# Kernel optimization log

Hardware: AMD Instinct MI355X
Metric: run time of the kernel (lower is better)

## Reference

```python
import jax, jax.numpy as jnp
import numpy as np

# HRR ops (holoformer): bind = circular convolution via FFT; unbind = circular
# correlation (bind with the approximate inverse), i.e. conj in freq domain.

def _fft(a):
    return jnp.fft.fft(a, axis=-1)

def _bind_f(Fa, Fb):
    return jnp.fft.ifft(Fa * Fb, axis=-1).real

def _unbind_f(Fs, Fk):
    return jnp.fft.ifft(Fs * jnp.conj(Fk), axis=-1).real


def setup_inputs() -> dict:
    key = jax.random.key(0)
    B, S, D = 4, 4096, 1024
    ks = jax.random.split(key, 5)
    scale = 1.0 / np.sqrt(D)
    inp = {
        "x": jax.random.normal(ks[0], (B, S, D), dtype=jnp.float32),
        "Wq": jax.random.normal(ks[1], (D, D), dtype=jnp.float32) * scale,
        "bq": jnp.zeros((D,), jnp.float32),
        "Wk": jax.random.normal(ks[2], (D, D), dtype=jnp.float32) * scale,
        "bk": jnp.zeros((D,), jnp.float32),
        "Wv": jax.random.normal(ks[3], (D, D), dtype=jnp.float32) * scale,
        "bv": jnp.zeros((D,), jnp.float32),
        "Wr": jax.random.normal(ks[4], (D, D), dtype=jnp.float32) * scale,
        "br": jnp.zeros((D,), jnp.float32),
    }
    return inp


def reference(x, Wq, bq, Wk, bk, Wv, bv, Wr, br):
    # tanh-gated linear projections (nn.Linear stores weight as [out, in])
    query = jnp.tanh(jnp.einsum('bsd,ed->bse', x, Wq) + bq)
    keys = jnp.tanh(jnp.einsum('bsd,ed->bse', x, Wk) + bk)
    values = jnp.tanh(jnp.einsum('bsd,ed->bse', x, Wv) + bv)
    remove_query = jnp.tanh(jnp.einsum('bsd,ed->bse', x, Wr) + br)

    # bind(keys, values) and sum over sequence -> s: (B, 1, D)
    x_k = _bind_f(_fft(keys), _fft(values))
    s = x_k.sum(axis=1, keepdims=True)
    Fs = _fft(s)

    # retrieve with query, add
    retrieved = _unbind_f(Fs, _fft(query))
    out = x + retrieved

    # remove: bind(remove_query, unbind(s, remove_query))
    Fr = _fft(remove_query)
    remove_values = _unbind_f(Fs, Fr)
    removes = _bind_f(Fr, _fft(remove_values))
    out = out - removes
    return out
```

## Files before the change

kernel.cpp:

```cpp
#include <hip/hip_runtime.h>
#include <hip/hip_fp16.h>

#define D 1024
#define LOG2D 10
#define S_LEN 4096
#define BATCH 4
#define NROWS (BATCH * S_LEN)
#define PI_F 3.14159265358979323846f

#define SLOT(p) ((p) + ((p) >> 4))
#define FBUF 1088
#define NTW 341

typedef _Float16 f16x8 __attribute__((ext_vector_type(8)));
typedef float f32x4 __attribute__((ext_vector_type(4)));

__device__ __forceinline__ float2 cmul(float2 a, float2 b) {
    return make_float2(a.x * b.x - a.y * b.y, a.x * b.y + a.y * b.x);
}

__device__ __forceinline__ float fast_tanh(float v) {
    float e = __expf(2.0f * v);
    return 1.0f - 2.0f * __builtin_amdgcn_rcpf(e + 1.0f);
}

__device__ __forceinline__ void g2lds16(const void* g, void* l) {
    __builtin_amdgcn_global_load_lds(
        (const __attribute__((address_space(1))) unsigned int*)g,
        (__attribute__((address_space(3))) unsigned int*)l, 16, 0, 0);
}

__global__ __launch_bounds__(256) void convert_all(
    const float* __restrict__ x,
    const float* __restrict__ w0, const float* __restrict__ w1,
    const float* __restrict__ w2, const float* __restrict__ w3,
    __half* __restrict__ xh,
    __half* __restrict__ h0, __half* __restrict__ h1,
    __half* __restrict__ h2, __half* __restrict__ h3)
{
    const int b = blockIdx.x;
    const float* s;
    __half* d;
    int li;
    if (b < 16384) { s = x; d = xh; li = b; }
    else {
        int t = b - 16384;
        int r = t >> 10;
        li = t & 1023;
        s = (r == 0) ? w0 : (r == 1) ? w1 : (r == 2) ? w2 : w3;
        d = (r == 0) ? h0 : (r == 1) ? h1 : (r == 2) ? h2 : h3;
    }
    const int idx = li * 256 + threadIdx.x;
    float4 v = ((const float4*)s)[idx];
    __half2 lo = __floats2half2_rn(v.x, v.y);
    __half2 hi = __floats2half2_rn(v.z, v.w);
    ((__half2*)d)[2 * idx + 0] = lo;
    ((__half2*)d)[2 * idx + 1] = hi;
}

__global__ __launch_bounds__(256) void gemm_mfma(
    const __half* __restrict__ Xh,
    const __half* __restrict__ WA, const float* __restrict__ bA, __half* __restrict__ OA,
    const __half* __restrict__ WB, const float* __restrict__ bB, __half* __restrict__ OB)
{
    const __half* W    = blockIdx.z ? WB : WA;
    const float* bias  = blockIdx.z ? bB : bA;
    __half* O          = blockIdx.z ? OB : OA;

    const int m0 = blockIdx.y * 128;
    const int n0 = blockIdx.x * 128;

    __shared__ __align__(16) __half As[128 * 32];
    __shared__ __align__(16) __half Bs[128 * 32];

    const int tid = threadIdx.x;
    const int wave = tid >> 6;
    const int lane = tid & 63;

    const int srow = lane >> 2;
    const int schunk = (lane & 3) ^ ((lane >> 3) & 3);

    const __half* gA[2];
    const __half* gB[2];
    __half* lA[2];
    __half* lB[2];
#pragma unroll
    for (int c = 0; c < 2; ++c) {
        const int rg = (wave * 2 + c) * 16 + srow;
        gA[c] = Xh + (size_t)(m0 + rg) * 1024 + schunk * 8;
        gB[c] = W  + (size_t)(n0 + rg) * 1024 + schunk * 8;
        lA[c] = As + (wave * 2 + c) * 512;
        lB[c] = Bs + (wave * 2 + c) * 512;
    }

    const int wm = (wave & 1) * 64;
    const int wn = (wave >> 1) * 64;
    const int quad = lane >> 4;
    const int l15 = lane & 15;

    int aoff[4], boff[4];
#pragma unroll
    for (int i = 0; i < 4; ++i) {
        const int Ra = wm + i * 16 + l15;
        aoff[i] = Ra * 32 + (quad ^ ((Ra >> 1) & 3)) * 8;
        const int Rb = wn + i * 16 + l15;
        boff[i] = Rb * 32 + (quad ^ ((Rb >> 1) & 3)) * 8;
    }

    f32x4 acc[4][4];
#pragma unroll
    for (int i = 0; i < 4; ++i)
#pragma unroll
        for (int j = 0; j < 4; ++j) acc[i][j] = (f32x4){0.f, 0.f, 0.f, 0.f};

    for (int kt = 0; kt < 32; ++kt) {
        const int kh = kt * 32;
        __syncthreads();
        g2lds16(gA[0] + kh, lA[0]);
        g2lds16(gA[1] + kh, lA[1]);
        g2lds16(gB[0] + kh, lB[0]);
        g2lds16(gB[1] + kh, lB[1]);
        __syncthreads();

        f16x8 af[4], bf[4];
#pragma unroll
        for (int i = 0; i < 4; ++i) af[i] = *(const f16x8*)(As + aoff[i]);
#pragma unroll
        for (int j = 0; j < 4; ++j) bf[j] = *(const f16x8*)(Bs + boff[j]);
#pragma unroll
        for (int i = 0; i < 4; ++i)
#pragma unroll
            for (int j = 0; j < 4; ++j)
                acc[i][j] = __builtin_amdgcn_mfma_f32_16x16x32_f16(af[i], bf[j], acc[i][j], 0, 0, 0);
    }

#pragma unroll
    for (int j = 0; j < 4; ++j) {
        const int n = n0 + wn + j * 16 + l15;
        const float bv = bias[n];
#pragma unroll
        for (int i = 0; i < 4; ++i) {
            const int mbase = m0 + wm + i * 16 + quad * 4;
#pragma unroll
            for (int r = 0; r < 4; ++r) {
                float v = fast_tanh(acc[i][j][r] + bv);
                O[(size_t)(mbase + r) * 1024 + n] = __float2half(v);
            }
        }
    }
}

__device__ __forceinline__ void build_twiddles_r4(float2* Wts, int tid) {
    for (int j = tid; j < NTW; j += 256) {
        int k, m;
        if (j == 0)      { k = 0;      m = 1;   }
        else if (j < 5)  { k = j - 1;  m = 4;   }
        else if (j < 21) { k = j - 5;  m = 16;  }
        else if (j < 85) { k = j - 21; m = 64;  }
        else             { k = j - 85; m = 256; }
        float ang = PI_F * (float)k / (2.0f * (float)m);
        Wts[j] = make_float2(cosf(ang), -sinf(ang));
    }
}

__device__ void fft1024_r4(float2* bufA, float2* bufB, const float2* Wts,
                           float dir, int tid) {
    float2* src = bufA;
    float2* dst = bufB;
    int m = 1;
#pragma unroll
    for (int s = 0; s < 5; ++s) {
        __syncthreads();
        const int k = tid & (m - 1);
        const int jb = tid >> (2 * s);
        float2 x0 = src[SLOT(tid)];
        float2 x1 = src[SLOT(tid + 256)];
        float2 x2 = src[SLOT(tid + 512)];
        float2 x3 = src[SLOT(tid + 768)];
        float2 y1, y2, y3;
        if (s == 0) { y1 = x1; y2 = x2; y3 = x3; }
        else {
            const int soff = (m - 1) / 3;
            float2 t1 = Wts[soff + k];
            t1.y *= dir;
            float2 t2 = cmul(t1, t1);
            float2 t3 = cmul(t1, t2);
            y1 = cmul(x1, t1);
            y2 = cmul(x2, t2);
            y3 = cmul(x3, t3);
        }
        float2 a = make_float2(x0.x + y2.x, x0.y + y2.y);
        float2 b = make_float2(x0.x - y2.x, x0.y - y2.y);
        float2 c = make_float2(y1.x + y3.x, y1.y + y3.y);
        float2 d = make_float2(y1.x - y3.x, y1.y - y3.y);
        float2 e = make_float2(dir * d.y, -dir * d.x);
        const int o = (jb << (2 * s + 2)) + k;
        dst[SLOT(o)]         = make_float2(a.x + c.x, a.y + c.y);
        dst[SLOT(o + m)]     = make_float2(b.x + e.x, b.y + e.y);
        dst[SLOT(o + 2 * m)] = make_float2(a.x - c.x, a.y - c.y);
        dst[SLOT(o + 3 * m)] = make_float2(b.x - e.x, b.y - e.y);
        float2* t = src; src = dst; dst = t;
        m <<= 2;
    }
    __syncthreads();
}

#define ROWS_PER_BLOCK 8
__global__ __launch_bounds__(256) void bind_accum_kernel(
    const __half* __restrict__ K, const __half* __restrict__ V, float2* __restrict__ Fs)
{
    __shared__ __align__(16) float2 bufA[FBUF];
    __shared__ __align__(16) float2 bufB[FBUF];
    __shared__ __align__(16) float2 Wts[NTW];
    const int tid = threadIdx.x;
    build_twiddles_r4(Wts, tid);

    const int row0 = blockIdx.x * ROWS_PER_BLOCK;
    const int b = row0 >> 12;

    float2 accr[4];
#pragma unroll
    for (int h = 0; h < 4; ++h) accr[h] = make_float2(0.f, 0.f);

    for (int r = 0; r < ROWS_PER_BLOCK; ++r) {
        const size_t base = (size_t)(row0 + r) * D;
#pragma unroll
        for (int h = 0; h < 4; ++h) {
            const int j = tid + (h << 8);
            bufA[SLOT(j)] = make_float2(__half2float(K[base + j]), __half2float(V[base + j]));
        }
        fft1024_r4(bufA, bufB, Wts, 1.0f, tid);
#pragma unroll
        for (int h = 0; h < 4; ++h) {
            const int j = tid + (h << 8);
            const int j2 = (D - j) & (D - 1);
            float2 Zt = bufB[SLOT(j)];
            float2 Zc = bufB[SLOT(j2)]; Zc.y = -Zc.y;
            float2 Fk = make_float2(0.5f * (Zt.x + Zc.x), 0.5f * (Zt.y + Zc.y));
            float2 Fv = make_float2(0.5f * (Zt.y - Zc.y), -0.5f * (Zt.x - Zc.x));
            float2 P = cmul(Fk, Fv);
            accr[h].x += P.x; accr[h].y += P.y;
        }
    }
#pragma unroll
    for (int h = 0; h < 4; ++h) {
        const int j = tid + (h << 8);
        atomicAdd(&Fs[(size_t)b * D + j].x, accr[h].x);
        atomicAdd(&Fs[(size_t)b * D + j].y, accr[h].y);
    }
}

__global__ __launch_bounds__(256) void retrieve_kernel(
    const __half* __restrict__ Q, const __half* __restrict__ R,
    const float2* __restrict__ Fs, const float* __restrict__ x, float* __restrict__ out)
{
    __shared__ __align__(16) float2 bufA[FBUF];
    __shared__ __align__(16) float2 bufB[FBUF];
    __shared__ __align__(16) float2 Wts[NTW];
    const int tid = threadIdx.x;
    build_twiddles_r4(Wts, tid);

    const int row = blockIdx.x;
    const int b = row >> 12;
    const size_t base = (size_t)row * D;

#pragma unroll
    for (int h = 0; h < 4; ++h) {
        const int j = tid + (h << 8);
        bufA[SLOT(j)] = make_float2(__half2float(Q[base + j]), __half2float(R[base + j]));
    }
    fft1024_r4(bufA, bufB, Wts, 1.0f, tid);

#pragma unroll
    for (int h = 0; h < 4; ++h) {
        const int j = tid + (h << 8);
        const int j2 = (D - j) & (D - 1);
        float2 Zt = bufB[SLOT(j)];
        float2 Zc = bufB[SLOT(j2)]; Zc.y = -Zc.y;
        float2 Fq = make_float2(0.5f * (Zt.x + Zc.x), 0.5f * (Zt.y + Zc.y));
        float2 Fr = make_float2(0.5f * (Zt.y - Zc.y), -0.5f * (Zt.x - Zc.x));
        float2 g  = make_float2(Fq.x - (Fr.x * Fr.x + Fr.y * Fr.y), -Fq.y);
        float2 Ff = Fs[(size_t)b * D + j];
        bufA[SLOT(j)] = cmul(Ff, g);
    }
    fft1024_r4(bufA, bufB, Wts, -1.0f, tid);

    const float inv = 1.0f / (float)D;
#pragma unroll
    for (int h = 0; h < 4; ++h) {
        const int j = tid + (h << 8);
        out[base + j] = x[base + j] + bufB[SLOT(j)].x * inv;
    }
}

extern "C" void kernel_launch(void* const* d_in, const int* in_sizes, int n_in,
                              void* d_out, int out_size, void* d_ws, size_t ws_size,
                              hipStream_t stream) {
    const float* x  = (const float*)d_in[0];
    const float* Wq = (const float*)d_in[1];
    const float* bq = (const float*)d_in[2];
    const float* Wk = (const float*)d_in[3];
    const float* bk = (const float*)d_in[4];
    const float* Wv = (const float*)d_in[5];
    const float* bv = (const float*)d_in[6];
    const float* Wr = (const float*)d_in[7];
    const float* br = (const float*)d_in[8];
    float* out = (float*)d_out;

    __half* P0 = (__half*)d_ws;
    __half* P1 = (__half*)((char*)d_ws + (size_t)NROWS * D * 2);
    float2* Fs = (float2*)((char*)d_ws + (size_t)NROWS * D * 4);

    __half* Xh  = (__half*)d_out;
    __half* Whk = (__half*)d_out + (size_t)16 * 1024 * 1024;
    __half* Whv = Whk + (size_t)1024 * 1024;
    __half* Whq = Whv + (size_t)1024 * 1024;
    __half* Whr = Whq + (size_t)1024 * 1024;

    convert_all<<<16384 + 4 * 1024, 256, 0, stream>>>(
        x, Wk, Wv, Wq, Wr, Xh, Whk, Whv, Whq, Whr);

    hipMemsetAsync(Fs, 0, (size_t)BATCH * D * sizeof(float2), stream);

    dim3 ggrid(1024 / 128, NROWS / 128, 2);
    gemm_mfma<<<ggrid, 256, 0, stream>>>(Xh, Whk, bk, P0, Whv, bv, P1);
    bind_accum_kernel<<<NROWS / ROWS_PER_BLOCK, 256, 0, stream>>>(P0, P1, Fs);
    gemm_mfma<<<ggrid, 256, 0, stream>>>(Xh, Whq, bq, P0, Whr, br, P1);
    retrieve_kernel<<<NROWS, 256, 0, stream>>>(P0, P1, Fs, x, out);
}
```

Measured before the change: 496.7 us.

## Fuse paired projection GEMMs to share X tile and remap blocks per XCD

Each GEMM block now computes both weight projections for the same 128x128 tile, so the X (A) tile is loaded into LDS once and reused for two MFMA accumulator sets, halving A-side global traffic. Block indices are remapped so each XCD handles a contiguous band of rows, which is meant to improve L2 locality of the X rows. The cost is doubled accumulator registers (128 floats) and more LDS per block, with launch_bounds(256,2), which may cause spills or lower occupancy.

```diff
diff --git a/kernel.cpp b/kernel.cpp
--- a/kernel.cpp
+++ b/kernel.cpp
@@ -58,20 +58,20 @@
     ((__half2*)d)[2 * idx + 1] = hi;
 }
 
-__global__ __launch_bounds__(256) void gemm_mfma(
+__global__ __launch_bounds__(256, 2) void gemm_mfma2(
     const __half* __restrict__ Xh,
-    const __half* __restrict__ WA, const float* __restrict__ bA, __half* __restrict__ OA,
-    const __half* __restrict__ WB, const float* __restrict__ bB, __half* __restrict__ OB)
+    const __half* __restrict__ W0, const float* __restrict__ b0, __half* __restrict__ O0,
+    const __half* __restrict__ W1, const float* __restrict__ b1, __half* __restrict__ O1)
 {
-    const __half* W    = blockIdx.z ? WB : WA;
-    const float* bias  = blockIdx.z ? bB : bA;
-    __half* O          = blockIdx.z ? OB : OA;
-
-    const int m0 = blockIdx.y * 128;
-    const int n0 = blockIdx.x * 128;
+    const int idx = blockIdx.x;
+    const int xcd = idx & 7;
+    const int j = idx >> 3;
+    const int n0 = (j & 7) * 128;
+    const int m0 = (xcd * 16 + (j >> 3)) * 128;
 
     __shared__ __align__(16) __half As[128 * 32];
-    __shared__ __align__(16) __half Bs[128 * 32];
+    __shared__ __align__(16) __half B0s[128 * 32];
+    __shared__ __align__(16) __half B1s[128 * 32];
 
     const int tid = threadIdx.x;
     const int wave = tid >> 6;
@@ -81,16 +81,20 @@
     const int schunk = (lane & 3) ^ ((lane >> 3) & 3);
 
     const __half* gA[2];
-    const __half* gB[2];
+    const __half* gB0[2];
+    const __half* gB1[2];
     __half* lA[2];
-    __half* lB[2];
+    __half* lB0[2];
+    __half* lB1[2];
 #pragma unroll
     for (int c = 0; c < 2; ++c) {
         const int rg = (wave * 2 + c) * 16 + srow;
-        gA[c] = Xh + (size_t)(m0 + rg) * 1024 + schunk * 8;
-        gB[c] = W  + (size_t)(n0 + rg) * 1024 + schunk * 8;
-        lA[c] = As + (wave * 2 + c) * 512;
-        lB[c] = Bs + (wave * 2 + c) * 512;
+        gA[c]  = Xh + (size_t)(m0 + rg) * 1024 + schunk * 8;
+        gB0[c] = W0 + (size_t)(n0 + rg) * 1024 + schunk * 8;
+        gB1[c] = W1 + (size_t)(n0 + rg) * 1024 + schunk * 8;
+        lA[c]  = As  + (wave * 2 + c) * 512;
+        lB0[c] = B0s + (wave * 2 + c) * 512;
+        lB1[c] = B1s + (wave * 2 + c) * 512;
     }
 
     const int wm = (wave & 1) * 64;
@@ -107,44 +111,55 @@
         boff[i] = Rb * 32 + (quad ^ ((Rb >> 1) & 3)) * 8;
     }
 
-    f32x4 acc[4][4];
+    f32x4 acc0[4][4], acc1[4][4];
 #pragma unroll
     for (int i = 0; i < 4; ++i)
 #pragma unroll
-        for (int j = 0; j < 4; ++j) acc[i][j] = (f32x4){0.f, 0.f, 0.f, 0.f};
+        for (int jj = 0; jj < 4; ++jj) {
+            acc0[i][jj] = (f32x4){0.f, 0.f, 0.f, 0.f};
+            acc1[i][jj] = (f32x4){0.f, 0.f, 0.f, 0.f};
+        }
 
     for (int kt = 0; kt < 32; ++kt) {
         const int kh = kt * 32;
         __syncthreads();
         g2lds16(gA[0] + kh, lA[0]);
         g2lds16(gA[1] + kh, lA[1]);
-        g2lds16(gB[0] + kh, lB[0]);
-        g2lds16(gB[1] + kh, lB[1]);
+        g2lds16(gB0[0] + kh, lB0[0]);
+        g2lds16(gB0[1] + kh, lB0[1]);
+        g2lds16(gB1[0] + kh, lB1[0]);
+        g2lds16(gB1[1] + kh, lB1[1]);
         __syncthreads();
 
-        f16x8 af[4], bf[4];
+        f16x8 af[4], bf0[4], bf1[4];
 #pragma unroll
         for (int i = 0; i < 4; ++i) af[i] = *(const f16x8*)(As + aoff[i]);
 #pragma unroll
-        for (int j = 0; j < 4; ++j) bf[j] = *(const f16x8*)(Bs + boff[j]);
+        for (int jj = 0; jj < 4; ++jj) {
+            bf0[jj] = *(const f16x8*)(B0s + boff[jj]);
+            bf1[jj] = *(const f16x8*)(B1s + boff[jj]);
+        }
 #pragma unroll
         for (int i = 0; i < 4; ++i)
 #pragma unroll
-            for (int j = 0; j < 4; ++j)
-                acc[i][j] = __builtin_amdgcn_mfma_f32_16x16x32_f16(af[i], bf[j], acc[i][j], 0, 0, 0);
-    }
-
-#pragma unroll
-    for (int j = 0; j < 4; ++j) {
-        const int n = n0 + wn + j * 16 + l15;
-        const float bv = bias[n];
+            for (int jj = 0; jj < 4; ++jj) {
+                acc0[i][jj] = __builtin_amdgcn_mfma_f32_16x16x32_f16(af[i], bf0[jj], acc0[i][jj], 0, 0, 0);
+                acc1[i][jj] = __builtin_amdgcn_mfma_f32_16x16x32_f16(af[i], bf1[jj], acc1[i][jj], 0, 0, 0);
+            }
+    }
+
+#pragma unroll
+    for (int jj = 0; jj < 4; ++jj) {
+        const int n = n0 + wn + jj * 16 + l15;
+        const float bv0 = b0[n];
+        const float bv1 = b1[n];
 #pragma unroll
         for (int i = 0; i < 4; ++i) {
             const int mbase = m0 + wm + i * 16 + quad * 4;
 #pragma unroll
             for (int r = 0; r < 4; ++r) {
-                float v = fast_tanh(acc[i][j][r] + bv);
-                O[(size_t)(mbase + r) * 1024 + n] = __float2half(v);
+                O0[(size_t)(mbase + r) * 1024 + n] = __float2half(fast_tanh(acc0[i][jj][r] + bv0));
+                O1[(size_t)(mbase + r) * 1024 + n] = __float2half(fast_tanh(acc1[i][jj][r] + bv1));
             }
         }
     }
@@ -322,9 +337,8 @@
 
     hipMemsetAsync(Fs, 0, (size_t)BATCH * D * sizeof(float2), stream);
 
-    dim3 ggrid(1024 / 128, NROWS / 128, 2);
-    gemm_mfma<<<ggrid, 256, 0, stream>>>(Xh, Whk, bk, P0, Whv, bv, P1);
+    gemm_mfma2<<<1024, 256, 0, stream>>>(Xh, Whk, bk, P0, Whv, bv, P1);
     bind_accum_kernel<<<NROWS / ROWS_PER_BLOCK, 256, 0, stream>>>(P0, P1, Fs);
-    gemm_mfma<<<ggrid, 256, 0, stream>>>(Xh, Whq, bq, P0, Whr, br, P1);
+    gemm_mfma2<<<1024, 256, 0, stream>>>(Xh, Whq, bq, P0, Whr, br, P1);
     retrieve_kernel<<<NROWS, 256, 0, stream>>>(P0, P1, Fs, x, out);
 }
```

New measurement: 472.3 us. -4.9%, faster.
